# Kernel tuning notes

Hardware: AMD Instinct MI355X
Metric: run time of the kernel (lower is better)

Reference implementation:

```python
import jax, jax.numpy as jnp
import numpy as np

NUM_HEADS = 16
D_MODEL = 1024
HEAD_DIM = D_MODEL // NUM_HEADS
SCALE = 8.0 / HEAD_DIM  # use_mup=True
LN_EPS = 1e-5


def setup_inputs() -> dict:
    key = jax.random.key(0)
    ks = jax.random.split(key, 8)
    B, N, M = 2, 2048, 2048
    std = 1.0 / np.sqrt(D_MODEL)
    return {
        "x1": jax.random.normal(ks[0], (B, N, D_MODEL), jnp.float32),
        "x2": jax.random.normal(ks[1], (B, M, D_MODEL), jnp.float32),
        "Wq": jax.random.normal(ks[2], (D_MODEL, D_MODEL), jnp.float32) * std,
        "Wk": jax.random.normal(ks[3], (D_MODEL, D_MODEL), jnp.float32) * std,
        "Wv": jax.random.normal(ks[4], (D_MODEL, D_MODEL), jnp.float32) * std,
        "Wp": jax.random.normal(ks[5], (D_MODEL, D_MODEL), jnp.float32) * std,
        "bp": jnp.zeros((D_MODEL,), jnp.float32),
        "ln_g": jnp.ones((HEAD_DIM,), jnp.float32),
        "ln_b": jnp.zeros((HEAD_DIM,), jnp.float32),
    }


def _layernorm(x, g, b):
    # LayerNorm over last dim (head_dim), eps=1e-5, biased variance (torch default)
    mu = jnp.mean(x, axis=-1, keepdims=True)
    var = jnp.mean(jnp.square(x - mu), axis=-1, keepdims=True)
    return (x - mu) * jax.lax.rsqrt(var + LN_EPS) * g + b


def reference(x1, x2, Wq, Wk, Wv, Wp, bp, ln_g, ln_b):
    B, N, C = x1.shape
    M = x2.shape[1]
    H, D = NUM_HEADS, HEAD_DIM
    # torch Linear: y = x @ W.T  (no qkv bias); reshape to [B, H, L, D]
    q = (x1 @ Wq.T).reshape(B, N, H, D).transpose(0, 2, 1, 3)
    k = (x2 @ Wk.T).reshape(B, M, H, D).transpose(0, 2, 1, 3)
    v = (x2 @ Wv.T).reshape(B, M, H, D).transpose(0, 2, 1, 3)
    # per-head QK LayerNorm (shared params)
    q = _layernorm(q, ln_g, ln_b)
    k = _layernorm(k, ln_g, ln_b)
    q = q * SCALE
    attn = jnp.einsum("bhnd,bhmd->bhnm", q, k)
    attn = jax.nn.softmax(attn, axis=-1)  # causal=False, attn_drop=0
    out = jnp.einsum("bhnm,bhmd->bhnd", attn, v)
    out = out.transpose(0, 2, 1, 3).reshape(B, N, C)
    return out @ Wp.T + bp
```

## Files before the change

### kernel.cpp

```cpp
#include <hip/hip_runtime.h>

#define DEV static __device__ __forceinline__

using bf16x8 = __attribute__((ext_vector_type(8))) short;
using f32x4  = __attribute__((ext_vector_type(4))) float;
using f32x16 = __attribute__((ext_vector_type(16))) float;

DEV unsigned short f2bf(float f) {
  union { float f; unsigned u; } v; v.f = f;
  return (unsigned short)((v.u + 0x7fffu + ((v.u >> 16) & 1u)) >> 16);
}
DEV unsigned pk2(float lo, float hi) {
  return (unsigned)f2bf(lo) | ((unsigned)f2bf(hi) << 16);
}
DEV unsigned cvtpk(float lo, float hi) {
  unsigned r;
  asm("v_cvt_pk_bf16_f32 %0, %1, %2" : "=v"(r) : "v"(lo), "v"(hi));
  return r;
}
DEV void pl32swap(unsigned &a, unsigned &b) {
  asm("v_permlane32_swap_b32 %0, %1" : "+v"(a), "+v"(b));
}
DEV bf16x8 mk8(unsigned a, unsigned b, unsigned c, unsigned d) {
  union { unsigned u[4]; bf16x8 v; } t;
  t.u[0] = a; t.u[1] = b; t.u[2] = c; t.u[3] = d;
  return t.v;
}
DEV f32x4 mfma16(bf16x8 a, bf16x8 b, f32x4 c) {
  return __builtin_amdgcn_mfma_f32_16x16x32_bf16(a, b, c, 0, 0, 0);
}
DEV f32x16 mfma32(bf16x8 a, bf16x8 b, f32x16 c) {
  return __builtin_amdgcn_mfma_f32_32x32x16_bf16(a, b, c, 0, 0, 0);
}
DEV f32x16 zero16() {
  f32x16 z;
#pragma unroll
  for (int i = 0; i < 16; ++i) z[i] = 0.f;
  return z;
}

typedef const __attribute__((address_space(1))) unsigned int* gas1;
typedef __attribute__((address_space(3))) unsigned int* las3;
DEV void gl16(const void* g, void* l) {
  __builtin_amdgcn_global_load_lds((gas1)g, (las3)l, 16, 0, 0);
}

__global__ __launch_bounds__(256, 8)
void conv_bf16(const float* __restrict__ x1, const float* __restrict__ x2,
               const float* __restrict__ Wq, const float* __restrict__ Wk,
               const float* __restrict__ Wv, const float* __restrict__ Wp,
               unsigned short* __restrict__ o)
{
  size_t e = ((size_t)blockIdx.x * 256 + threadIdx.x) * 8;
  const float* s; size_t off;
  if (e < 4194304u)       { s = x1; off = e; }
  else if (e < 8388608u)  { s = x2; off = e - 4194304u; }
  else if (e < 9437184u)  { s = Wq; off = e - 8388608u; }
  else if (e < 10485760u) { s = Wk; off = e - 9437184u; }
  else if (e < 11534336u) { s = Wv; off = e - 10485760u; }
  else                    { s = Wp; off = e - 11534336u; }
  const float4* p = reinterpret_cast<const float4*>(s + off);
  float4 a = p[0], b = p[1];
  int4 r;
  r.x = (int)cvtpk(a.x, a.y); r.y = (int)cvtpk(a.z, a.w);
  r.z = (int)cvtpk(b.x, b.y); r.w = (int)cvtpk(b.z, b.w);
  *reinterpret_cast<int4*>(o + e) = r;
}

__global__ __launch_bounds__(256, 2)
void gemm_qkv_bf(const unsigned short* __restrict__ xb,
                 const float* __restrict__ lg, const float* __restrict__ lb,
                 unsigned short* __restrict__ qb, unsigned short* __restrict__ kb,
                 unsigned short* __restrict__ vtb)
{
  __shared__ short As[128 * 64];
  __shared__ short Bs[128 * 64];
  const int tid = threadIdx.x;
  const int l = tid & 63, w = tid >> 6;
  const int wr = w >> 1, wc = w & 1;
  const int z = blockIdx.z;
  const unsigned short* A = (z == 0) ? xb : (xb + 4194304);
  const unsigned short* W = xb + 8388608 + (size_t)z * 1048576;
  const int brow = blockIdx.y * 128, bcol = blockIdx.x * 128;

  const f32x4 zero = {0.f, 0.f, 0.f, 0.f};
  f32x4 acc[4][4];
#pragma unroll
  for (int mi = 0; mi < 4; ++mi)
#pragma unroll
    for (int ni = 0; ni < 4; ++ni) acc[mi][ni] = zero;

  const int srow = w * 32 + (l >> 3);
  const int scol = (l & 7) * 8;

  for (int kt = 0; kt < 16; ++kt) {
    const unsigned short* ga = A + (size_t)(brow + srow) * 1024 + kt * 64 + scol;
    const unsigned short* gb = W + (size_t)(bcol + srow) * 1024 + kt * 64 + scol;
#pragma unroll
    for (int i = 0; i < 4; ++i) {
      gl16(ga + (size_t)i * 8 * 1024, &As[(w * 32 + i * 8) * 64]);
      gl16(gb + (size_t)i * 8 * 1024, &Bs[(w * 32 + i * 8) * 64]);
    }
    __syncthreads();
#pragma unroll
    for (int kk = 0; kk < 2; ++kk) {
      const int k0 = kk * 32 + ((l >> 4) << 3);
      bf16x8 af[4], bfr[4];
#pragma unroll
      for (int mi = 0; mi < 4; ++mi)
        af[mi] = *reinterpret_cast<const bf16x8*>(
            &As[((wr << 6) + (mi << 4) + (l & 15)) * 64 + k0]);
#pragma unroll
      for (int ni = 0; ni < 4; ++ni)
        bfr[ni] = *reinterpret_cast<const bf16x8*>(
            &Bs[((wc << 6) + (ni << 4) + (l & 15)) * 64 + k0]);
#pragma unroll
      for (int mi = 0; mi < 4; ++mi)
#pragma unroll
        for (int ni = 0; ni < 4; ++ni)
          acc[mi][ni] = mfma16(af[mi], bfr[ni], acc[mi][ni]);
    }
    __syncthreads();
  }

  if (z < 2) {
    unsigned short* dst = (z == 0) ? qb : kb;
    const float scl = (z == 0) ? 0.18033688011112042f : 1.0f;
    const int h = blockIdx.x * 2 + wc;
    float gw4[4], bw4[4];
#pragma unroll
    for (int ni = 0; ni < 4; ++ni) {
      gw4[ni] = lg[ni * 16 + (l & 15)] * scl;
      bw4[ni] = lb[ni * 16 + (l & 15)] * scl;
    }
#pragma unroll
    for (int mi = 0; mi < 4; ++mi) {
      float ylo[4];
#pragma unroll
      for (int r = 0; r < 4; ++r) {
        float v0 = acc[mi][0][r], v1 = acc[mi][1][r];
        float v2 = acc[mi][2][r], v3 = acc[mi][3][r];
        float s  = (v0 + v1) + (v2 + v3);
        float s2 = (v0 * v0 + v1 * v1) + (v2 * v2 + v3 * v3);
#pragma unroll
        for (int off = 1; off < 16; off <<= 1) {
          s  += __shfl_xor(s, off);
          s2 += __shfl_xor(s2, off);
        }
        float mean = s * (1.f / 64.f);
        float var  = s2 * (1.f / 64.f) - mean * mean;
        float rstd = rsqrtf(var + 1e-5f);
        float y[4];
        y[0] = (v0 - mean) * rstd * gw4[0] + bw4[0];
        y[1] = (v1 - mean) * rstd * gw4[1] + bw4[1];
        y[2] = (v2 - mean) * rstd * gw4[2] + bw4[2];
        y[3] = (v3 - mean) * rstd * gw4[3] + bw4[3];
        if (!(r & 1)) {
          ylo[0] = y[0]; ylo[1] = y[1]; ylo[2] = y[2]; ylo[3] = y[3];
        } else {
          int rowg0 = brow + (wr << 6) + (mi << 4) + ((l >> 4) << 2) + r - 1;
          int b = rowg0 >> 11, n = rowg0 & 2047;
          unsigned short* base =
              dst + (((size_t)(b * 16 + h) << 11) + n) * 64 + (l & 15);
#pragma unroll
          for (int ni = 0; ni < 4; ++ni) {
            unsigned u = cvtpk(ylo[ni], y[ni]);
            base[ni * 16]      = (unsigned short)(u & 0xffffu);
            base[ni * 16 + 64] = (unsigned short)(u >> 16);
          }
        }
      }
    }
  } else {
    const int bb = brow >> 11;
    const int nblk = brow & 2047;
#pragma unroll
    for (int mi = 0; mi < 4; ++mi)
#pragma unroll
      for (int ni = 0; ni < 4; ++ni) {
        int n0 = nblk + (wr << 6) + (mi << 4) + ((l >> 4) << 2);
        int colg = bcol + (wc << 6) + (ni << 4) + (l & 15);
        int h = colg >> 6, d = colg & 63;
        unsigned u0 = cvtpk(acc[mi][ni][0], acc[mi][ni][1]);
        unsigned u1 = cvtpk(acc[mi][ni][2], acc[mi][ni][3]);
        int2 u; u.x = (int)u0; u.y = (int)u1;
        *reinterpret_cast<int2*>(
            &vtb[((size_t)(bb * 16 + h) * 64 + d) * 2048 + n0]) = u;
      }
  }
}

__global__ __launch_bounds__(256, 2)
void attn_fwd(const unsigned short* __restrict__ Q,
              const unsigned short* __restrict__ K,
              const unsigned short* __restrict__ Vt,
              unsigned short* __restrict__ O)
{
  __shared__ short Ks[2][64 * 64];
  __shared__ short Vs[2][64 * 64];
  const int tid = threadIdx.x, w = tid >> 6, l = tid & 63;
  const int lo5 = l & 31, hi = l >> 5;
  const int bh = blockIdx.y;
  const int qbase = blockIdx.x * 128 + w * 32;
  const unsigned short* Qg = Q + ((size_t)bh * 2048 + qbase) * 64;
  const unsigned short* Kg = K + (size_t)bh * 2048 * 64;
  const unsigned short* Vg = Vt + (size_t)bh * 64 * 2048;

  bf16x8 qf[4];
#pragma unroll
  for (int ks = 0; ks < 4; ++ks)
    qf[ks] = *reinterpret_cast<const bf16x8*>(Qg + lo5 * 64 + ks * 16 + hi * 8);

  f32x16 oc0 = zero16(), oc1 = zero16();
  float lsum = 0.f;

  const int srow = tid >> 3;
  const int sc8 = (tid & 7) * 8;
  const int swz0 = sc8 ^ ((srow & 7) * 8);

  int4 ka0, ka1, va0, va1;
  ka0 = *reinterpret_cast<const int4*>(Kg + srow * 64 + sc8);
  ka1 = *reinterpret_cast<const int4*>(Kg + (32 + srow) * 64 + sc8);
  va0 = *reinterpret_cast<const int4*>(Vg + (size_t)srow * 2048 + sc8);
  va1 = *reinterpret_cast<const int4*>(Vg + (size_t)(32 + srow) * 2048 + sc8);
  *reinterpret_cast<int4*>(&Ks[0][(srow << 6) + swz0]) = ka0;
  *reinterpret_cast<int4*>(&Ks[0][((32 + srow) << 6) + swz0]) = ka1;
  *reinterpret_cast<int4*>(&Vs[0][(srow << 6) + swz0]) = va0;
  *reinterpret_cast<int4*>(&Vs[0][((32 + srow) << 6) + swz0]) = va1;
  __syncthreads();

  const unsigned short* kp = Kg + 4096 + srow * 64 + sc8;
  const unsigned short* vp = Vg + 64 + (size_t)srow * 2048 + sc8;

  for (int it = 0; it < 32; ++it) {
    const int cur = it & 1;
    const short* Kc = Ks[cur];
    const short* Vc = Vs[cur];

    if (it < 31) {
      ka0 = *reinterpret_cast<const int4*>(kp);
      ka1 = *reinterpret_cast<const int4*>(kp + 2048);
      va0 = *reinterpret_cast<const int4*>(vp);
      va1 = *reinterpret_cast<const int4*>(vp + 65536);
      kp += 4096; vp += 64;
    }

    f32x16 s0 = zero16(), s1 = zero16();
    __builtin_amdgcn_s_setprio(1);
#pragma unroll
    for (int ks = 0; ks < 4; ++ks) {
      const int colc = (16 * ks + 8 * hi) ^ ((lo5 & 7) << 3);
      bf16x8 k0 = *reinterpret_cast<const bf16x8*>(&Kc[(lo5 << 6) + colc]);
      s0 = mfma32(k0, qf[ks], s0);
      bf16x8 k1 = *reinterpret_cast<const bf16x8*>(&Kc[((32 + lo5) << 6) + colc]);
      s1 = mfma32(k1, qf[ks], s1);
    }
    __builtin_amdgcn_s_setprio(0);

    auto pvsub = [&](const f32x16& sv, int jbase) {
      float p0[16];
#pragma unroll
      for (int r = 0; r < 16; ++r) p0[r] = exp2f(sv[r]);
      lsum += (((p0[0] + p0[1]) + (p0[2] + p0[3])) +
               ((p0[4] + p0[5]) + (p0[6] + p0[7]))) +
              (((p0[8] + p0[9]) + (p0[10] + p0[11])) +
               ((p0[12] + p0[13]) + (p0[14] + p0[15])));
#pragma unroll
      for (int f = 0; f < 2; ++f) {
        unsigned x  = cvtpk(p0[8 * f + 0], p0[8 * f + 1]);
        unsigned zz = cvtpk(p0[8 * f + 2], p0[8 * f + 3]);
        unsigned y  = cvtpk(p0[8 * f + 4], p0[8 * f + 5]);
        unsigned ww = cvtpk(p0[8 * f + 6], p0[8 * f + 7]);
        pl32swap(x, y);
        pl32swap(zz, ww);
        bf16x8 pa = mk8(x, zz, y, ww);
        const int colc = (jbase + 16 * f + 8 * hi);
        bf16x8 v0 = *reinterpret_cast<const bf16x8*>(
            &Vc[(lo5 << 6) + (colc ^ ((lo5 & 7) << 3))]);
        bf16x8 v1 = *reinterpret_cast<const bf16x8*>(
            &Vc[((32 + lo5) << 6) + (colc ^ ((lo5 & 7) << 3))]);
        __builtin_amdgcn_s_setprio(1);
        oc0 = mfma32(pa, v0, oc0);
        oc1 = mfma32(pa, v1, oc1);
        __builtin_amdgcn_s_setprio(0);
      }
    };
    pvsub(s0, 0);
    pvsub(s1, 32);

    if (it < 31) {
      const int nb = cur ^ 1;
      *reinterpret_cast<int4*>(&Ks[nb][(srow << 6) + swz0]) = ka0;
      *reinterpret_cast<int4*>(&Ks[nb][((32 + srow) << 6) + swz0]) = ka1;
      *reinterpret_cast<int4*>(&Vs[nb][(srow << 6) + swz0]) = va0;
      *reinterpret_cast<int4*>(&Vs[nb][((32 + srow) << 6) + swz0]) = va1;
    }
    __syncthreads();
  }

  lsum += __shfl_xor(lsum, 32);
  float inv = 1.f / lsum;
  unsigned short* Og = O + ((size_t)(bh >> 4) * 2048 + qbase) * 1024 + (bh & 15) * 64;
#pragma unroll
  for (int r = 0; r < 16; ++r) {
    int qrow = (r & 3) + 8 * (r >> 2) + 4 * hi;
    float ir = __shfl(inv, qrow);
    Og[qrow * 1024 + lo5]      = f2bf(oc0[r] * ir);
    Og[qrow * 1024 + 32 + lo5] = f2bf(oc1[r] * ir);
  }
}

__global__ __launch_bounds__(256, 2)
void gemm_out_bf(const unsigned short* __restrict__ ob,
                 const unsigned short* __restrict__ wpb,
                 const float* __restrict__ bp, float* __restrict__ out)
{
  __shared__ short As[128 * 64];
  __shared__ short Bs[128 * 64];
  const int tid = threadIdx.x;
  const int l = tid & 63, w = tid >> 6;
  const int wr = w >> 1, wc = w & 1;
  const int brow = blockIdx.y * 128, bcol = blockIdx.x * 128;

  const f32x4 zero = {0.f, 0.f, 0.f, 0.f};
  f32x4 acc[4][4];
#pragma unroll
  for (int mi = 0; mi < 4; ++mi)
#pragma unroll
    for (int ni = 0; ni < 4; ++ni) acc[mi][ni] = zero;

  const int srow = w * 32 + (l >> 3);
  const int scol = (l & 7) * 8;

  for (int kt = 0; kt < 16; ++kt) {
    const unsigned short* ga = ob + (size_t)(brow + srow) * 1024 + kt * 64 + scol;
    const unsigned short* gb = wpb + (size_t)(bcol + srow) * 1024 + kt * 64 + scol;
#pragma unroll
    for (int i = 0; i < 4; ++i) {
      gl16(ga + (size_t)i * 8 * 1024, &As[(w * 32 + i * 8) * 64]);
      gl16(gb + (size_t)i * 8 * 1024, &Bs[(w * 32 + i * 8) * 64]);
    }
    __syncthreads();
#pragma unroll
    for (int kk = 0; kk < 2; ++kk) {
      const int k0 = kk * 32 + ((l >> 4) << 3);
      bf16x8 af[4], bfr[4];
#pragma unroll
      for (int mi = 0; mi < 4; ++mi)
        af[mi] = *reinterpret_cast<const bf16x8*>(
            &As[((wr << 6) + (mi << 4) + (l & 15)) * 64 + k0]);
#pragma unroll
      for (int ni = 0; ni < 4; ++ni)
        bfr[ni] = *reinterpret_cast<const bf16x8*>(
            &Bs[((wc << 6) + (ni << 4) + (l & 15)) * 64 + k0]);
#pragma unroll
      for (int mi = 0; mi < 4; ++mi)
#pragma unroll
        for (int ni = 0; ni < 4; ++ni)
          acc[mi][ni] = mfma16(af[mi], bfr[ni], acc[mi][ni]);
    }
    __syncthreads();
  }

  float bias[4];
#pragma unroll
  for (int ni = 0; ni < 4; ++ni)
    bias[ni] = bp[bcol + (wc << 6) + (ni << 4) + (l & 15)];
#pragma unroll
  for (int mi = 0; mi < 4; ++mi)
#pragma unroll
    for (int ni = 0; ni < 4; ++ni)
#pragma unroll
      for (int r = 0; r < 4; ++r) {
        int rowg = brow + (wr << 6) + (mi << 4) + ((l >> 4) << 2) + r;
        int colg = bcol + (wc << 6) + (ni << 4) + (l & 15);
        out[(size_t)rowg * 1024 + colg] = acc[mi][ni][r] + bias[ni];
      }
}

extern "C" void kernel_launch(void* const* d_in, const int* in_sizes, int n_in,
                              void* d_out, int out_size, void* d_ws, size_t ws_size,
                              hipStream_t stream)
{
  const float* x1 = (const float*)d_in[0];
  const float* x2 = (const float*)d_in[1];
  const float* Wq = (const float*)d_in[2];
  const float* Wk = (const float*)d_in[3];
  const float* Wv = (const float*)d_in[4];
  const float* Wp = (const float*)d_in[5];
  const float* bp = (const float*)d_in[6];
  const float* lg = (const float*)d_in[7];
  const float* lb = (const float*)d_in[8];

  char* wsb = (char*)d_ws;
  unsigned short* xb   = (unsigned short*)wsb;
  unsigned short* qb   = (unsigned short*)(wsb + 25165824);
  unsigned short* kb   = qb + 4194304;
  unsigned short* vtb  = kb + 4194304;
  unsigned short* obuf = vtb + 4194304;
  float* out = (float*)d_out;

  conv_bf16<<<6144, 256, 0, stream>>>(x1, x2, Wq, Wk, Wv, Wp, xb);
  gemm_qkv_bf<<<dim3(8, 32, 3), 256, 0, stream>>>(xb, lg, lb, qb, kb, vtb);
  attn_fwd<<<dim3(16, 32), 256, 0, stream>>>(qb, kb, vtb, obuf);
  gemm_out_bf<<<dim3(8, 32), 256, 0, stream>>>(obuf,
      xb + 11534336, bp, out);
}
```

Baseline: 134.4 us.

## Halve attention block size, swizzle GEMM tile order, use native exp2

The attention kernel now launches 128-thread blocks covering 64 queries each, doubling the grid to 1024 blocks. Each thread loads four K/V rows per tile instead of two, so a block still stages a full 64x64 tile. Both GEMMs remap block IDs so consecutive blocks walk down the M dimension, aiming for better L2 reuse of weight tiles. The softmax exponent uses the raw amdgcn exp2 builtin to avoid libm overhead. The trade-off is that each K/V tile is loaded by twice as many blocks in total, for better occupancy and wave balance.

```diff
diff --git a/kernel.cpp b/kernel.cpp
--- a/kernel.cpp
+++ b/kernel.cpp
@@ -5,6 +5,12 @@
 using bf16x8 = __attribute__((ext_vector_type(8))) short;
 using f32x4  = __attribute__((ext_vector_type(4))) float;
 using f32x16 = __attribute__((ext_vector_type(16))) float;
+
+#if __has_builtin(__builtin_amdgcn_exp2f)
+#define EXP2(x) __builtin_amdgcn_exp2f(x)
+#else
+#define EXP2(x) exp2f(x)
+#endif
 
 DEV unsigned short f2bf(float f) {
   union { float f; unsigned u; } v; v.f = f;
@@ -81,7 +87,10 @@
   const int z = blockIdx.z;
   const unsigned short* A = (z == 0) ? xb : (xb + 4194304);
   const unsigned short* W = xb + 8388608 + (size_t)z * 1048576;
-  const int brow = blockIdx.y * 128, bcol = blockIdx.x * 128;
+  const int id = blockIdx.x + (blockIdx.y << 3);
+  const int tl = ((id & 7) << 5) | (id >> 3);
+  const int bx = tl & 7, by = tl >> 3;
+  const int brow = by * 128, bcol = bx * 128;
 
   const f32x4 zero = {0.f, 0.f, 0.f, 0.f};
   f32x4 acc[4][4];
@@ -126,7 +135,7 @@
   if (z < 2) {
     unsigned short* dst = (z == 0) ? qb : kb;
     const float scl = (z == 0) ? 0.18033688011112042f : 1.0f;
-    const int h = blockIdx.x * 2 + wc;
+    const int h = bx * 2 + wc;
     float gw4[4], bw4[4];
 #pragma unroll
     for (int ni = 0; ni < 4; ++ni) {
@@ -190,7 +199,7 @@
   }
 }
 
-__global__ __launch_bounds__(256, 2)
+__global__ __launch_bounds__(128)
 void attn_fwd(const unsigned short* __restrict__ Q,
               const unsigned short* __restrict__ K,
               const unsigned short* __restrict__ Vt,
@@ -201,7 +210,7 @@
   const int tid = threadIdx.x, w = tid >> 6, l = tid & 63;
   const int lo5 = l & 31, hi = l >> 5;
   const int bh = blockIdx.y;
-  const int qbase = blockIdx.x * 128 + w * 32;
+  const int qbase = blockIdx.x * 64 + w * 32;
   const unsigned short* Qg = Q + ((size_t)bh * 2048 + qbase) * 64;
   const unsigned short* Kg = K + (size_t)bh * 2048 * 64;
   const unsigned short* Vg = Vt + (size_t)bh * 64 * 2048;
@@ -216,17 +225,25 @@
 
   const int srow = tid >> 3;
   const int sc8 = (tid & 7) * 8;
-  const int swz0 = sc8 ^ ((srow & 7) * 8);
-
-  int4 ka0, ka1, va0, va1;
-  ka0 = *reinterpret_cast<const int4*>(Kg + srow * 64 + sc8);
-  ka1 = *reinterpret_cast<const int4*>(Kg + (32 + srow) * 64 + sc8);
-  va0 = *reinterpret_cast<const int4*>(Vg + (size_t)srow * 2048 + sc8);
-  va1 = *reinterpret_cast<const int4*>(Vg + (size_t)(32 + srow) * 2048 + sc8);
-  *reinterpret_cast<int4*>(&Ks[0][(srow << 6) + swz0]) = ka0;
-  *reinterpret_cast<int4*>(&Ks[0][((32 + srow) << 6) + swz0]) = ka1;
-  *reinterpret_cast<int4*>(&Vs[0][(srow << 6) + swz0]) = va0;
-  *reinterpret_cast<int4*>(&Vs[0][((32 + srow) << 6) + swz0]) = va1;
+  const int swz = sc8 ^ ((srow & 7) << 3);
+
+  int4 ka0, ka1, ka2, ka3, va0, va1, va2, va3;
+  ka0 = *reinterpret_cast<const int4*>(Kg + (srow)      * 64 + sc8);
+  ka1 = *reinterpret_cast<const int4*>(Kg + (srow + 16) * 64 + sc8);
+  ka2 = *reinterpret_cast<const int4*>(Kg + (srow + 32) * 64 + sc8);
+  ka3 = *reinterpret_cast<const int4*>(Kg + (srow + 48) * 64 + sc8);
+  va0 = *reinterpret_cast<const int4*>(Vg + (size_t)(srow)      * 2048 + sc8);
+  va1 = *reinterpret_cast<const int4*>(Vg + (size_t)(srow + 16) * 2048 + sc8);
+  va2 = *reinterpret_cast<const int4*>(Vg + (size_t)(srow + 32) * 2048 + sc8);
+  va3 = *reinterpret_cast<const int4*>(Vg + (size_t)(srow + 48) * 2048 + sc8);
+  *reinterpret_cast<int4*>(&Ks[0][((srow)      << 6) + swz]) = ka0;
+  *reinterpret_cast<int4*>(&Ks[0][((srow + 16) << 6) + swz]) = ka1;
+  *reinterpret_cast<int4*>(&Ks[0][((srow + 32) << 6) + swz]) = ka2;
+  *reinterpret_cast<int4*>(&Ks[0][((srow + 48) << 6) + swz]) = ka3;
+  *reinterpret_cast<int4*>(&Vs[0][((srow)      << 6) + swz]) = va0;
+  *reinterpret_cast<int4*>(&Vs[0][((srow + 16) << 6) + swz]) = va1;
+  *reinterpret_cast<int4*>(&Vs[0][((srow + 32) << 6) + swz]) = va2;
+  *reinterpret_cast<int4*>(&Vs[0][((srow + 48) << 6) + swz]) = va3;
   __syncthreads();
 
   const unsigned short* kp = Kg + 4096 + srow * 64 + sc8;
@@ -239,9 +256,13 @@
 
     if (it < 31) {
       ka0 = *reinterpret_cast<const int4*>(kp);
-      ka1 = *reinterpret_cast<const int4*>(kp + 2048);
+      ka1 = *reinterpret_cast<const int4*>(kp + 1024);
+      ka2 = *reinterpret_cast<const int4*>(kp + 2048);
+      ka3 = *reinterpret_cast<const int4*>(kp + 3072);
       va0 = *reinterpret_cast<const int4*>(vp);
-      va1 = *reinterpret_cast<const int4*>(vp + 65536);
+      va1 = *reinterpret_cast<const int4*>(vp + 32768);
+      va2 = *reinterpret_cast<const int4*>(vp + 65536);
+      va3 = *reinterpret_cast<const int4*>(vp + 98304);
       kp += 4096; vp += 64;
     }
 
@@ -260,7 +281,7 @@
     auto pvsub = [&](const f32x16& sv, int jbase) {
       float p0[16];
 #pragma unroll
-      for (int r = 0; r < 16; ++r) p0[r] = exp2f(sv[r]);
+      for (int r = 0; r < 16; ++r) p0[r] = EXP2(sv[r]);
       lsum += (((p0[0] + p0[1]) + (p0[2] + p0[3])) +
                ((p0[4] + p0[5]) + (p0[6] + p0[7]))) +
               (((p0[8] + p0[9]) + (p0[10] + p0[11])) +
@@ -290,10 +311,14 @@
 
     if (it < 31) {
       const int nb = cur ^ 1;
-      *reinterpret_cast<int4*>(&Ks[nb][(srow << 6) + swz0]) = ka0;
-      *reinterpret_cast<int4*>(&Ks[nb][((32 + srow) << 6) + swz0]) = ka1;
-      *reinterpret_cast<int4*>(&Vs[nb][(srow << 6) + swz0]) = va0;
-      *reinterpret_cast<int4*>(&Vs[nb][((32 + srow) << 6) + swz0]) = va1;
+      *reinterpret_cast<int4*>(&Ks[nb][((srow)      << 6) + swz]) = ka0;
+      *reinterpret_cast<int4*>(&Ks[nb][((srow + 16) << 6) + swz]) = ka1;
+      *reinterpret_cast<int4*>(&Ks[nb][((srow + 32) << 6) + swz]) = ka2;
+      *reinterpret_cast<int4*>(&Ks[nb][((srow + 48) << 6) + swz]) = ka3;
+      *reinterpret_cast<int4*>(&Vs[nb][((srow)      << 6) + swz]) = va0;
+      *reinterpret_cast<int4*>(&Vs[nb][((srow + 16) << 6) + swz]) = va1;
+      *reinterpret_cast<int4*>(&Vs[nb][((srow + 32) << 6) + swz]) = va2;
+      *reinterpret_cast<int4*>(&Vs[nb][((srow + 48) << 6) + swz]) = va3;
     }
     __syncthreads();
   }
@@ -320,7 +345,9 @@
   const int tid = threadIdx.x;
   const int l = tid & 63, w = tid >> 6;
   const int wr = w >> 1, wc = w & 1;
-  const int brow = blockIdx.y * 128, bcol = blockIdx.x * 128;
+  const int id = blockIdx.x + (blockIdx.y << 3);
+  const int tl = ((id & 7) << 5) | (id >> 3);
+  const int brow = (tl >> 3) * 128, bcol = (tl & 7) * 128;
 
   const f32x4 zero = {0.f, 0.f, 0.f, 0.f};
   f32x4 acc[4][4];
@@ -402,7 +429,7 @@
 
   conv_bf16<<<6144, 256, 0, stream>>>(x1, x2, Wq, Wk, Wv, Wp, xb);
   gemm_qkv_bf<<<dim3(8, 32, 3), 256, 0, stream>>>(xb, lg, lb, qb, kb, vtb);
-  attn_fwd<<<dim3(16, 32), 256, 0, stream>>>(qb, kb, vtb, obuf);
+  attn_fwd<<<dim3(32, 32), 128, 0, stream>>>(qb, kb, vtb, obuf);
   gemm_out_bf<<<dim3(8, 32), 256, 0, stream>>>(obuf,
       xb + 11534336, bp, out);
 }
```

Result: faster. 130.3 us (-3.1%).
